# Kernel tuning notes

Measured on AMD Instinct MI355X. Metric: run time of the kernel, lower is better.

Reference implementation:

```python
import jax, jax.numpy as jnp
import numpy as np

B, S, D, H = 16, 512, 768, 12
DH = D // H


def setup_inputs() -> dict:
    key = jax.random.key(0)
    ks = jax.random.split(key, 12)
    hidden_states = jax.random.normal(ks[0], (B, S, D), dtype=jnp.float32)
    # additive padding mask: 0 for valid, -10000 for padded tail tokens
    lengths = jax.random.randint(ks[1], (B,), S // 2, S + 1)
    pad = (jnp.arange(S)[None, :] >= lengths[:, None]).astype(jnp.float32)
    attention_mask = (pad * -10000.0)[:, None, None, :]  # [B,1,1,S]
    # row-stochastic graph prior over codes
    pr = jax.random.uniform(ks[2], (B, S, S), dtype=jnp.float32)
    prior = pr / jnp.sum(pr, axis=-1, keepdims=True)
    s = 0.02
    params = dict(
        Wq=jax.random.normal(ks[3], (D, D)) * s, bq=jnp.zeros((D,)),
        Wk=jax.random.normal(ks[4], (D, D)) * s, bk=jnp.zeros((D,)),
        Wv=jax.random.normal(ks[5], (D, D)) * s, bv=jnp.zeros((D,)),
        Wg=jax.random.normal(ks[6], (D, 2)) * s, bg=jnp.zeros((2,)),
        Wo=jax.random.normal(ks[7], (D, D)) * s, bo=jnp.zeros((D,)),
        gamma=jnp.ones((D,)), beta=jnp.zeros((D,)),
    )
    return dict(hidden_states=hidden_states, attention_mask=attention_mask,
                prior=prior, **params)


def _layer_norm(x, gamma, beta, eps=1e-5):
    mu = jnp.mean(x, axis=-1, keepdims=True)
    var = jnp.mean(jnp.square(x - mu), axis=-1, keepdims=True)
    return (x - mu) * jax.lax.rsqrt(var + eps) * gamma + beta


def reference(hidden_states, attention_mask, prior,
              Wq, bq, Wk, bk, Wv, bv, Wg, bg, Wo, bo, gamma, beta):
    b, s, d = hidden_states.shape
    # project and split heads: [B,S,H,DH]
    q = (hidden_states @ Wq + bq).reshape(b, s, H, DH)
    k = (hidden_states @ Wk + bk).reshape(b, s, H, DH)
    v = (hidden_states @ Wv + bv).reshape(b, s, H, DH)
    scores = jnp.einsum('bshd,bthd->bhst', q, k) / jnp.sqrt(jnp.float32(DH))
    scores = scores + attention_mask  # broadcast [B,1,1,S]
    probs = jax.nn.softmax(scores, axis=-1)  # [B,H,S,S]
    # gate: avg-pool over valid tokens, softmax(linear/2)
    valid = (attention_mask.squeeze((1, 2)) == 0.0).astype(hidden_states.dtype)  # [B,S]
    denom = jnp.maximum(jnp.sum(valid, axis=1, keepdims=True), 1.0)
    h_pool = jnp.sum(hidden_states * valid[:, :, None], axis=1) / denom  # [B,D]
    gate = jax.nn.softmax((h_pool @ Wg + bg) / 2.0, axis=-1)  # [B,2]
    probs = probs * gate[:, 0, None, None, None] + prior[:, None, :, :] * gate[:, 1, None, None, None]
    ctx = jnp.einsum('bhst,bthd->bshd', probs, v).reshape(b, s, d)
    out = jax.nn.relu(ctx @ Wo + bo)
    out = _layer_norm(out + hidden_states, gamma, beta)
    return out
```

## Files before the change

kernel.cpp:

```cpp
#include <hip/hip_runtime.h>

#define NB_ 16
#define S_ 512
#define D_ 768
#define H_ 12
#define DH_ 64
#define QT_ 64
#define KT_ 128
#define LDQ_ 1536

typedef __attribute__((ext_vector_type(8))) short bf16x8;
typedef __attribute__((ext_vector_type(4))) float f32x4;
typedef unsigned short ushort_t;

__device__ __forceinline__ unsigned short f2bf(float f){
  unsigned int u = __float_as_uint(f);
  u += 0x7fffu + ((u >> 16) & 1u);
  return (unsigned short)(u >> 16);
}
__device__ __forceinline__ float bf2f(unsigned short s){
  return __uint_as_float(((unsigned int)s) << 16);
}
__device__ __forceinline__ unsigned int pack2(float a, float b){
  return (unsigned int)f2bf(a) | ((unsigned int)f2bf(b) << 16);
}
__device__ __forceinline__ void gld16(const ushort_t* g, ushort_t* l){
  __builtin_amdgcn_global_load_lds((const __attribute__((address_space(1))) unsigned int*)g,
                                   (__attribute__((address_space(3))) unsigned int*)l, 16, 0, 0);
}

__global__ __launch_bounds__(256) void k_setup(
    const float* __restrict__ hs, const float* __restrict__ mask, const float* __restrict__ prior,
    const float* __restrict__ W0, const float* __restrict__ W1,
    const float* __restrict__ W2, const float* __restrict__ W3,
    const float* __restrict__ b0, const float* __restrict__ b1, const float* __restrict__ b2,
    ushort_t* __restrict__ hsb, ushort_t* __restrict__ wt, float* __restrict__ bqkv,
    float* __restrict__ partial, float* __restrict__ pcnt, ushort_t* __restrict__ priorb)
{
  __shared__ float t[32][33];
  const int bx = blockIdx.x, tid = threadIdx.x;
  if (bx < 512){
    int chunk = bx & 31, b = bx >> 5;
    const float* mrow = mask + b * S_ + chunk * 16;
    const float* base = hs + ((size_t)b * S_ + chunk * 16) * D_;
    ushort_t* obase = hsb + ((size_t)b * S_ + chunk * 16) * D_;
    float a0 = 0.f, a1 = 0.f, a2 = 0.f, cnt = 0.f;
#pragma unroll 2
    for (int s = 0; s < 16; s++){
      const float* r = base + (size_t)s * D_;
      float x0 = r[tid], x1 = r[tid + 256], x2 = r[tid + 512];
      ushort_t* o = obase + (size_t)s * D_;
      o[tid] = f2bf(x0); o[tid + 256] = f2bf(x1); o[tid + 512] = f2bf(x2);
      if (mrow[s] == 0.0f){ a0 += x0; a1 += x1; a2 += x2; cnt += 1.0f; }
    }
    float* o = partial + (size_t)(b * 32 + chunk) * D_;
    o[tid] = a0; o[tid + 256] = a1; o[tid + 512] = a2;
    if (tid == 0) pcnt[b * 32 + chunk] = cnt;
  } else if (bx < 512 + 2304){
    int idx = bx - 512;
    int z = idx / 576, rem = idx - z * 576;
    int ky = rem / 24, nx = rem - ky * 24;
    const float* W = (z == 0) ? W0 : (z == 1) ? W1 : (z == 2) ? W2 : W3;
    ushort_t* o = wt + (size_t)z * D_ * D_;
    int j = tid & 31, i0 = tid >> 5;
    int kb = ky * 32, nb = nx * 32;
#pragma unroll
    for (int r = 0; r < 4; r++){
      int i = i0 + r * 8;
      t[i][j] = W[(size_t)(kb + i) * D_ + nb + j];
    }
    __syncthreads();
#pragma unroll
    for (int r = 0; r < 4; r++){
      int i = i0 + r * 8;
      o[(size_t)(nb + i) * D_ + kb + j] = f2bf(t[j][i]);
    }
  } else if (bx < 2825){
    int i = (bx - 2816) * 256 + tid;
    if (i < 3 * D_){
      float v = (i < D_) ? b0[i] : (i < 2 * D_) ? b1[i - D_] : b2[i - 2 * D_];
      bqkv[i] = v;
    }
  } else {
    size_t i = (size_t)(bx - 2825) * 4096 + (size_t)tid * 16;
    const float4* s4 = (const float4*)(prior + i);
    float4 f0 = s4[0], f1 = s4[1], f2 = s4[2], f3 = s4[3];
    uint4 p0, p1;
    p0.x = pack2(f0.x, f0.y); p0.y = pack2(f0.z, f0.w);
    p0.z = pack2(f1.x, f1.y); p0.w = pack2(f1.z, f1.w);
    p1.x = pack2(f2.x, f2.y); p1.y = pack2(f2.z, f2.w);
    p1.z = pack2(f3.x, f3.y); p1.w = pack2(f3.z, f3.w);
    *(uint4*)(priorb + i) = p0;
    *(uint4*)(priorb + i + 8) = p1;
  }
}

__global__ __launch_bounds__(256) void k_pool2(const float* __restrict__ partial, const float* __restrict__ pcnt,
                                               const float* __restrict__ Wg, const float* __restrict__ bg,
                                               float* __restrict__ gate){
  int b = blockIdx.x, tid = threadIdx.x;
  __shared__ float red[256];
  __shared__ float hp[768];
  float a0 = 0.f, a1 = 0.f, a2 = 0.f;
#pragma unroll
  for (int c = 0; c < 32; c++){
    const float* p = partial + (size_t)(b * 32 + c) * D_;
    a0 += p[tid]; a1 += p[tid + 256]; a2 += p[tid + 512];
  }
  float denom = 0.f;
#pragma unroll
  for (int c = 0; c < 32; c++) denom += pcnt[b * 32 + c];
  float inv = 1.0f / fmaxf(denom, 1.0f);
  hp[tid] = a0 * inv; hp[tid + 256] = a1 * inv; hp[tid + 512] = a2 * inv;
  __syncthreads();
  float p0 = 0.f, p1 = 0.f;
  for (int d = tid; d < D_; d += 256){ p0 += hp[d] * Wg[d * 2]; p1 += hp[d] * Wg[d * 2 + 1]; }
  red[tid] = p0; __syncthreads();
  for (int o = 128; o > 0; o >>= 1){ if (tid < o) red[tid] += red[tid + o]; __syncthreads(); }
  float z0 = red[0]; __syncthreads();
  red[tid] = p1; __syncthreads();
  for (int o = 128; o > 0; o >>= 1){ if (tid < o) red[tid] += red[tid + o]; __syncthreads(); }
  float z1 = red[0];
  if (tid == 0){
    z0 = (z0 + bg[0]) * 0.5f; z1 = (z1 + bg[1]) * 0.5f;
    float m = fmaxf(z0, z1);
    float e0 = __expf(z0 - m), e1 = __expf(z1 - m);
    float ssum = e0 + e1;
    gate[b * 2] = e0 / ssum; gate[b * 2 + 1] = e1 / ssum;
  }
}

template<int OUTBF16, int RELU, int RESID, int MAP, int VSPLIT>
__global__ __launch_bounds__(256, 2) void k_gemm_bt(
    const ushort_t* __restrict__ Am, long sA, int lda,
    const ushort_t* __restrict__ Bm, long sB, int ldb,
    void* __restrict__ Cp, long sC, int ldc, void* __restrict__ Cp2,
    const float* __restrict__ bias,
    const float* __restrict__ resid, float alpha, int K)
{
  __shared__ ushort_t As[2][128 * 64];
  __shared__ ushort_t Bs[2][128 * 64];
  int z, bm, bn;
  if (MAP == 2){ z = blockIdx.x; bm = blockIdx.y; bn = blockIdx.z; }
  else if (MAP == 1){ z = blockIdx.z; bm = blockIdx.x; bn = blockIdx.y; }
  else { z = blockIdx.z; bm = blockIdx.y; bn = blockIdx.x; }
  const ushort_t* Ab = Am + (size_t)z * sA;
  const ushort_t* Bb = Bm + (size_t)z * sB;
  const long coff = (long)z * sC;
  const int tid = threadIdx.x;
  const int m0 = bm * 128, n0 = bn * 128;
  const int wid = tid >> 6, lane = tid & 63;
  const int quad = lane >> 4, l16 = lane & 15;
  const int wm = wid >> 1, wn = wid & 1;
  const int sw = l16 & 7;

  auto stage = [&](int buf, int k0){
#pragma unroll
    for (int c = 0; c < 4; c++){
      int idx = tid + c * 256;
      int row = idx >> 3, p = idx & 7;
      int cg = p ^ (row & 7);
      gld16(Ab + (size_t)(m0 + row) * lda + k0 + cg * 8, &As[buf][idx * 8]);
    }
#pragma unroll
    for (int c = 0; c < 4; c++){
      int idx = tid + c * 256;
      int row = idx >> 3, p = idx & 7;
      int cg = p ^ (row & 7);
      gld16(Bb + (size_t)(n0 + row) * ldb + k0 + cg * 8, &Bs[buf][idx * 8]);
    }
  };

  f32x4 acc[4][4];
#pragma unroll
  for (int i = 0; i < 4; i++)
#pragma unroll
    for (int j = 0; j < 4; j++) acc[i][j] = (f32x4){0.f, 0.f, 0.f, 0.f};

  stage(0, 0);
  int cur = 0;
  for (int k0 = 0; k0 < K; k0 += 64){
    if (k0 + 64 < K){
      stage(cur ^ 1, k0 + 64);
      __builtin_amdgcn_sched_barrier(0);
      asm volatile("s_waitcnt vmcnt(8)" ::: "memory");
    } else {
      __builtin_amdgcn_sched_barrier(0);
      asm volatile("s_waitcnt vmcnt(0)" ::: "memory");
    }
    __builtin_amdgcn_sched_barrier(0);
    __builtin_amdgcn_s_barrier();
#pragma unroll
    for (int ks = 0; ks < 2; ks++){
      bf16x8 af[4], bfv[4];
#pragma unroll
      for (int mi = 0; mi < 4; mi++){
        int row = wm * 64 + mi * 16 + l16;
        af[mi] = *(const bf16x8*)(&As[cur][(row * 8 + ((ks * 4 + quad) ^ sw)) * 8]);
      }
#pragma unroll
      for (int ni = 0; ni < 4; ni++){
        int row = wn * 64 + ni * 16 + l16;
        bfv[ni] = *(const bf16x8*)(&Bs[cur][(row * 8 + ((ks * 4 + quad) ^ sw)) * 8]);
      }
      __builtin_amdgcn_s_setprio(1);
#pragma unroll
      for (int mi = 0; mi < 4; mi++)
#pragma unroll
        for (int ni = 0; ni < 4; ni++)
          acc[mi][ni] = __builtin_amdgcn_mfma_f32_16x16x32_bf16(af[mi], bfv[ni], acc[mi][ni], 0, 0, 0);
      __builtin_amdgcn_s_setprio(0);
    }
    __builtin_amdgcn_sched_barrier(0);
    __builtin_amdgcn_s_barrier();
    cur ^= 1;
  }

  if (VSPLIT && n0 >= 1536){
    ushort_t* vtp = (ushort_t*)Cp2;
    const int bb = m0 >> 9;
#pragma unroll
    for (int mi = 0; mi < 4; mi++){
#pragma unroll
      for (int ni = 0; ni < 4; ni++){
        int col = n0 + wn * 64 + ni * 16 + l16;
        float bcol = bias[col];
        int hh = (col - 1536) >> 6, dh = (col - 1536) & 63;
        int trow = (m0 & 511) + wm * 64 + mi * 16 + quad * 4;
        uint2 pk;
        pk.x = pack2(acc[mi][ni][0] + bcol, acc[mi][ni][1] + bcol);
        pk.y = pack2(acc[mi][ni][2] + bcol, acc[mi][ni][3] + bcol);
        *(uint2*)(vtp + ((size_t)(bb * H_ + hh) * DH_ + dh) * S_ + trow) = pk;
      }
    }
    return;
  }

#pragma unroll
  for (int mi = 0; mi < 4; mi++){
#pragma unroll
    for (int ni = 0; ni < 4; ni++){
      int col = n0 + wn * 64 + ni * 16 + l16;
      float bcol = bias ? bias[col] : 0.0f;
#pragma unroll
      for (int r = 0; r < 4; r++){
        int row = m0 + wm * 64 + mi * 16 + quad * 4 + r;
        float v = acc[mi][ni][r] * alpha + bcol;
        if (RELU) v = fmaxf(v, 0.0f);
        if (RESID) v += resid[(size_t)row * ldc + col];
        long idx = coff + (long)row * ldc + col;
        if (OUTBF16) ((ushort_t*)Cp)[idx] = f2bf(v);
        else         ((float*)Cp)[idx] = v;
      }
    }
  }
}

__global__ __launch_bounds__(256) void k_flash(
    const ushort_t* __restrict__ qkv,
    const ushort_t* __restrict__ vt,
    const ushort_t* __restrict__ priorctx,
    const float* __restrict__ mask,
    const float* __restrict__ gate,
    ushort_t* __restrict__ ctx)
{
  __shared__ ushort_t Ks[KT_ * 64];
  __shared__ ushort_t Vs[DH_ * 128];
  __shared__ ushort_t Ps[QT_ * 136];
  __shared__ float rs[QT_];
  const int z = blockIdx.x, b = z / H_, h = z - b * H_;
  const int q0 = blockIdx.y * QT_;
  const int tid = threadIdx.x;
  const int wid = tid >> 6, lane = tid & 63, quad = lane >> 4, l16 = lane & 15;

  bf16x8 bq[4][2];
#pragma unroll
  for (int ni = 0; ni < 4; ni++)
#pragma unroll
    for (int ks = 0; ks < 2; ks++)
      bq[ni][ks] = *(const bf16x8*)(qkv + ((size_t)(b * S_ + q0 + ni * 16 + l16)) * LDQ_
                                    + h * DH_ + ks * 32 + quad * 8);
  if (tid < QT_) rs[tid] = 0.f;

  f32x4 accv[4];
#pragma unroll
  for (int ni = 0; ni < 4; ni++) accv[ni] = (f32x4){0.f, 0.f, 0.f, 0.f};

  for (int t0 = 0; t0 < S_; t0 += KT_){
    if (mask[b * S_ + t0] != 0.0f) break;
#pragma unroll
    for (int c = 0; c < 4; c++){
      int idx = tid + c * 256;
      int row = idx >> 3, p = idx & 7;
      int cg = p ^ (row & 7);
      gld16(qkv + ((size_t)(b * S_ + t0 + row)) * LDQ_ + D_ + h * DH_ + cg * 8, &Ks[idx * 8]);
    }
#pragma unroll
    for (int c = 0; c < 4; c++){
      int idx = tid + c * 256;
      int row = idx >> 4, p = idx & 15;
      int cg = p ^ (row & 15);
      gld16(vt + (size_t)z * (DH_ * S_) + (size_t)row * S_ + t0 + cg * 8, &Vs[idx * 8]);
    }
    __syncthreads();

    f32x4 accs[2][4];
#pragma unroll
    for (int mi = 0; mi < 2; mi++)
#pragma unroll
      for (int ni = 0; ni < 4; ni++) accs[mi][ni] = (f32x4){0.f, 0.f, 0.f, 0.f};
#pragma unroll
    for (int ks = 0; ks < 2; ks++){
      bf16x8 ak[2];
#pragma unroll
      for (int mi = 0; mi < 2; mi++){
        int row = wid * 32 + mi * 16 + l16;
        ak[mi] = *(const bf16x8*)(&Ks[(row * 8 + ((ks * 4 + quad) ^ (l16 & 7))) * 8]);
      }
#pragma unroll
      for (int mi = 0; mi < 2; mi++)
#pragma unroll
        for (int ni = 0; ni < 4; ni++)
          accs[mi][ni] = __builtin_amdgcn_mfma_f32_16x16x32_bf16(ak[mi], bq[ni][ks], accs[mi][ni], 0, 0, 0);
    }

    float mv[2][4];
#pragma unroll
    for (int mi = 0; mi < 2; mi++)
#pragma unroll
      for (int r = 0; r < 4; r++)
        mv[mi][r] = mask[b * S_ + t0 + wid * 32 + mi * 16 + quad * 4 + r];
    float rowpart[4] = {0.f, 0.f, 0.f, 0.f};
#pragma unroll
    for (int mi = 0; mi < 2; mi++){
#pragma unroll
      for (int ni = 0; ni < 4; ni++){
        float e0 = __expf(accs[mi][ni][0] * 0.125f + mv[mi][0]);
        float e1 = __expf(accs[mi][ni][1] * 0.125f + mv[mi][1]);
        float e2 = __expf(accs[mi][ni][2] * 0.125f + mv[mi][2]);
        float e3 = __expf(accs[mi][ni][3] * 0.125f + mv[mi][3]);
        rowpart[ni] += (e0 + e1) + (e2 + e3);
        uint2 pk;
        pk.x = pack2(e0, e1);
        pk.y = pack2(e2, e3);
        *(uint2*)(&Ps[(ni * 16 + l16) * 136 + wid * 32 + mi * 16 + quad * 4]) = pk;
      }
    }
#pragma unroll
    for (int ni = 0; ni < 4; ni++){
      rowpart[ni] += __shfl_xor(rowpart[ni], 16);
      rowpart[ni] += __shfl_xor(rowpart[ni], 32);
    }
    if (lane < 16){
#pragma unroll
      for (int ni = 0; ni < 4; ni++) atomicAdd(&rs[ni * 16 + l16], rowpart[ni]);
    }
    __syncthreads();

#pragma unroll
    for (int ks = 0; ks < 4; ks++){
      bf16x8 ap = *(const bf16x8*)(&Ps[(wid * 16 + l16) * 136 + ks * 32 + quad * 8]);
#pragma unroll
      for (int ni = 0; ni < 4; ni++){
        bf16x8 bv8 = *(const bf16x8*)(&Vs[((ni * 16 + l16) * 16 + ((ks * 4 + quad) ^ l16)) * 8]);
        accv[ni] = __builtin_amdgcn_mfma_f32_16x16x32_bf16(ap, bv8, accv[ni], 0, 0, 0);
      }
    }
    __syncthreads();
  }

  const float g0 = gate[b * 2], g1 = gate[b * 2 + 1];
#pragma unroll
  for (int ni = 0; ni < 4; ni++){
#pragma unroll
    for (int r = 0; r < 4; r++){
      int q = wid * 16 + quad * 4 + r;
      int dh = ni * 16 + l16;
      float scl = g0 / rs[q];
      size_t idx = ((size_t)(b * S_ + q0 + q)) * D_ + h * DH_ + dh;
      float v = accv[ni][r] * scl + g1 * bf2f(priorctx[idx]);
      ctx[idx] = f2bf(v);
    }
  }
}

__global__ __launch_bounds__(256) void k_ln(float* __restrict__ out, const float* __restrict__ gamma,
                                            const float* __restrict__ beta){
  __shared__ float red[256];
  int row = blockIdx.x, tid = threadIdx.x;
  float* p = out + (size_t)row * D_;
  float x0 = p[tid], x1 = p[tid + 256], x2 = p[tid + 512];
  red[tid] = x0 + x1 + x2; __syncthreads();
  for (int o = 128; o > 0; o >>= 1){ if (tid < o) red[tid] += red[tid + o]; __syncthreads(); }
  float mu = red[0] * (1.0f / 768.0f);
  __syncthreads();
  float d0 = x0 - mu, d1 = x1 - mu, d2 = x2 - mu;
  red[tid] = d0 * d0 + d1 * d1 + d2 * d2; __syncthreads();
  for (int o = 128; o > 0; o >>= 1){ if (tid < o) red[tid] += red[tid + o]; __syncthreads(); }
  float rsv = rsqrtf(red[0] * (1.0f / 768.0f) + 1e-5f);
  p[tid]       = d0 * rsv * gamma[tid]       + beta[tid];
  p[tid + 256] = d1 * rsv * gamma[tid + 256] + beta[tid + 256];
  p[tid + 512] = d2 * rsv * gamma[tid + 512] + beta[tid + 512];
}

extern "C" void kernel_launch(void* const* d_in, const int* in_sizes, int n_in,
                              void* d_out, int out_size, void* d_ws, size_t ws_size,
                              hipStream_t stream){
  const float* hs    = (const float*)d_in[0];
  const float* mask  = (const float*)d_in[1];
  const float* prior = (const float*)d_in[2];
  const float* Wq = (const float*)d_in[3];  const float* bq = (const float*)d_in[4];
  const float* Wk = (const float*)d_in[5];  const float* bk = (const float*)d_in[6];
  const float* Wv = (const float*)d_in[7];  const float* bv = (const float*)d_in[8];
  const float* Wg = (const float*)d_in[9];  const float* bg = (const float*)d_in[10];
  const float* Wo = (const float*)d_in[11]; const float* bo = (const float*)d_in[12];
  const float* gamma = (const float*)d_in[13]; const float* beta = (const float*)d_in[14];
  float* out = (float*)d_out;

  size_t off = 0;
  auto alloc = [&](size_t bytes) -> char* {
    char* p = (char*)d_ws + off;
    off += (bytes + 255) & ~(size_t)255;
    return p;
  };
  const size_t HSD = (size_t)NB_ * S_ * D_;
  ushort_t* hsb     = (ushort_t*)alloc(HSD * 2);
  ushort_t* qkvb    = (ushort_t*)alloc(HSD * 2 * 2);
  ushort_t* vtb     = (ushort_t*)alloc(HSD * 2);
  ushort_t* wt      = (ushort_t*)alloc((size_t)4 * D_ * D_ * 2);
  ushort_t* priorctx= (ushort_t*)alloc(HSD * 2);
  ushort_t* ctx     = (ushort_t*)alloc(HSD * 2);
  float*    bqkv    = (float*)alloc((size_t)3 * D_ * 4);
  float*    gate    = (float*)alloc(256);
  float*    partial = (float*)alloc((size_t)NB_ * 32 * D_ * 4);
  float*    pcnt    = (float*)alloc((size_t)NB_ * 32 * 4);
  ushort_t* priorb  = ctx;

  k_setup<<<dim3(3849), 256, 0, stream>>>(hs, mask, prior, Wq, Wk, Wv, Wo, bq, bk, bv,
                                          hsb, wt, bqkv, partial, pcnt, priorb);
  k_pool2<<<dim3(NB_), 256, 0, stream>>>(partial, pcnt, Wg, bg, gate);
  k_gemm_bt<1, 0, 0, 1, 1><<<dim3(64, 18, 1), 256, 0, stream>>>(
      hsb, 0, D_, wt, 0, D_, qkvb, 0, LDQ_, vtb, bqkv, nullptr, 1.0f, D_);
  k_gemm_bt<1, 0, 0, 2, 0><<<dim3(16, 4, 6), 256, 0, stream>>>(
      priorb, (long)S_ * S_, S_, vtb, (long)H_ * DH_ * S_, S_,
      priorctx, (long)S_ * D_, D_, nullptr, nullptr, nullptr, 1.0f, S_);
  k_flash<<<dim3(NB_ * H_, S_ / QT_), 256, 0, stream>>>(
      qkvb, vtb, priorctx, mask, gate, ctx);
  k_gemm_bt<0, 1, 1, 1, 0><<<dim3(64, 6, 1), 256, 0, stream>>>(
      ctx, 0, D_, wt + 3 * (size_t)D_ * D_, 0, D_, out, 0, D_, nullptr, bo, hs, 1.0f, D_);
  k_ln<<<dim3(NB_ * S_), 256, 0, stream>>>(out, gamma, beta);
}
```

Baseline: 265.4 us.

## Replace QKV projection GEMM with 256x256-tile 8-wave pipelined kernel

```diff
diff --git a/kernel.cpp b/kernel.cpp
--- a/kernel.cpp
+++ b/kernel.cpp
@@ -256,6 +256,165 @@
   }
 }
 
+__global__ __launch_bounds__(512, 2) void k_gemm8_qkv(
+    const ushort_t* __restrict__ A,
+    const ushort_t* __restrict__ B,
+    ushort_t* __restrict__ Cq,
+    ushort_t* __restrict__ vt,
+    const float* __restrict__ bias)
+{
+  __shared__ ushort_t Al[2][2][256 * 32];
+  __shared__ ushort_t Bl[2][2][256 * 32];
+  const int tid = threadIdx.x;
+  const int m0 = blockIdx.x * 256, n0 = blockIdx.y * 256;
+  const int wid = tid >> 6, lane = tid & 63;
+  const int quad = lane >> 4, l16 = lane & 15;
+  const int wm = wid >> 2, wn = wid & 3;
+
+  const int i0c = tid, i1c = tid + 512;
+  const int r0 = i0c >> 2, c0 = (i0c & 3) ^ (r0 & 3);
+  const int r1 = i1c >> 2, c1 = (i1c & 3) ^ (r1 & 3);
+  const size_t a0 = (size_t)(m0 + r0) * 768 + c0 * 8;
+  const size_t a1 = (size_t)(m0 + r1) * 768 + c1 * 8;
+  const size_t b0 = (size_t)(n0 + r0) * 768 + c0 * 8;
+  const size_t b1 = (size_t)(n0 + r1) * 768 + c1 * 8;
+
+  auto stA = [&](int slot, int ks, int kt){
+    int ko = kt * 64 + ks * 32;
+    gld16(A + a0 + ko, &Al[slot][ks][i0c * 8]);
+    gld16(A + a1 + ko, &Al[slot][ks][i1c * 8]);
+  };
+  auto stB = [&](int slot, int ks, int kt){
+    int ko = kt * 64 + ks * 32;
+    gld16(B + b0 + ko, &Bl[slot][ks][i0c * 8]);
+    gld16(B + b1 + ko, &Bl[slot][ks][i1c * 8]);
+  };
+  auto rdA = [&](int slot, int ks, int mi) -> bf16x8 {
+    int row = wm * 128 + mi * 16 + l16;
+    return *(const bf16x8*)(&Al[slot][ks][(row * 4 + (quad ^ (row & 3))) * 8]);
+  };
+  auto rdB = [&](int slot, int ks, int ni) -> bf16x8 {
+    int row = wn * 64 + ni * 16 + l16;
+    return *(const bf16x8*)(&Bl[slot][ks][(row * 4 + (quad ^ (row & 3))) * 8]);
+  };
+
+  f32x4 acc[8][4];
+#pragma unroll
+  for (int i = 0; i < 8; i++)
+#pragma unroll
+    for (int j = 0; j < 4; j++) acc[i][j] = (f32x4){0.f, 0.f, 0.f, 0.f};
+
+  stA(0, 0, 0); stB(0, 0, 0); stA(0, 1, 0); stB(0, 1, 0);
+  stA(1, 0, 1); stB(1, 0, 1); stA(1, 1, 1);
+  __builtin_amdgcn_sched_barrier(0);
+  asm volatile("s_waitcnt vmcnt(6)" ::: "memory");
+  __builtin_amdgcn_sched_barrier(0);
+  __builtin_amdgcn_s_barrier();
+
+#pragma unroll 2
+  for (int t = 0; t < 12; ++t){
+    const int s = t & 1, o = s ^ 1;
+    bf16x8 aL[8], aH[8], bL[4], bH[4];
+#pragma unroll
+    for (int mi = 0; mi < 8; mi++) aL[mi] = rdA(s, 0, mi);
+#pragma unroll
+    for (int ni = 0; ni < 4; ni++) bL[ni] = rdB(s, 0, ni);
+    if (t + 1 < 12) stB(o, 1, t + 1);
+    __builtin_amdgcn_sched_barrier(0);
+    __builtin_amdgcn_s_barrier();
+    asm volatile("s_waitcnt lgkmcnt(0)" ::: "memory");
+    __builtin_amdgcn_sched_barrier(0);
+    __builtin_amdgcn_s_setprio(1);
+#pragma unroll
+    for (int mi = 0; mi < 4; mi++)
+#pragma unroll
+      for (int ni = 0; ni < 4; ni++)
+        acc[mi][ni] = __builtin_amdgcn_mfma_f32_16x16x32_bf16(aL[mi], bL[ni], acc[mi][ni], 0, 0, 0);
+    __builtin_amdgcn_s_setprio(0);
+    __builtin_amdgcn_sched_barrier(0);
+    __builtin_amdgcn_s_barrier();
+#pragma unroll
+    for (int ni = 0; ni < 4; ni++) bH[ni] = rdB(s, 1, ni);
+    if (t + 2 < 12) stA(s, 0, t + 2);
+    __builtin_amdgcn_sched_barrier(0);
+    __builtin_amdgcn_s_barrier();
+    asm volatile("s_waitcnt lgkmcnt(0)" ::: "memory");
+    __builtin_amdgcn_sched_barrier(0);
+    __builtin_amdgcn_s_setprio(1);
+#pragma unroll
+    for (int mi = 4; mi < 8; mi++)
+#pragma unroll
+      for (int ni = 0; ni < 4; ni++)
+        acc[mi][ni] = __builtin_amdgcn_mfma_f32_16x16x32_bf16(aL[mi], bL[ni], acc[mi][ni], 0, 0, 0);
+    __builtin_amdgcn_s_setprio(0);
+    __builtin_amdgcn_sched_barrier(0);
+    __builtin_amdgcn_s_barrier();
+#pragma unroll
+    for (int mi = 0; mi < 8; mi++) aH[mi] = rdA(s, 1, mi);
+    if (t + 2 < 12) stB(s, 0, t + 2);
+    __builtin_amdgcn_sched_barrier(0);
+    __builtin_amdgcn_s_barrier();
+    asm volatile("s_waitcnt lgkmcnt(0)" ::: "memory");
+    __builtin_amdgcn_sched_barrier(0);
+    __builtin_amdgcn_s_setprio(1);
+#pragma unroll
+    for (int mi = 0; mi < 4; mi++)
+#pragma unroll
+      for (int ni = 0; ni < 4; ni++)
+        acc[mi][ni] = __builtin_amdgcn_mfma_f32_16x16x32_bf16(aH[mi], bH[ni], acc[mi][ni], 0, 0, 0);
+    __builtin_amdgcn_s_setprio(0);
+    __builtin_amdgcn_sched_barrier(0);
+    __builtin_amdgcn_s_barrier();
+    if (t + 2 < 12) stA(s, 1, t + 2);
+    __builtin_amdgcn_sched_barrier(0);
+    __builtin_amdgcn_s_barrier();
+    __builtin_amdgcn_s_setprio(1);
+#pragma unroll
+    for (int mi = 4; mi < 8; mi++)
+#pragma unroll
+      for (int ni = 0; ni < 4; ni++)
+        acc[mi][ni] = __builtin_amdgcn_mfma_f32_16x16x32_bf16(aH[mi], bH[ni], acc[mi][ni], 0, 0, 0);
+    __builtin_amdgcn_s_setprio(0);
+    __builtin_amdgcn_sched_barrier(0);
+    if (t < 10) { asm volatile("s_waitcnt vmcnt(6)" ::: "memory"); }
+    else        { asm volatile("s_waitcnt vmcnt(0)" ::: "memory"); }
+    __builtin_amdgcn_sched_barrier(0);
+    __builtin_amdgcn_s_barrier();
+  }
+
+  if (n0 >= 1536){
+    const int bb = m0 >> 9;
+#pragma unroll
+    for (int mi = 0; mi < 8; mi++){
+#pragma unroll
+      for (int ni = 0; ni < 4; ni++){
+        int col = n0 + wn * 64 + ni * 16 + l16;
+        float bcol = bias[col];
+        int hh = (col - 1536) >> 6, dh = (col - 1536) & 63;
+        int trow = (m0 & 511) + wm * 128 + mi * 16 + quad * 4;
+        uint2 pk;
+        pk.x = pack2(acc[mi][ni][0] + bcol, acc[mi][ni][1] + bcol);
+        pk.y = pack2(acc[mi][ni][2] + bcol, acc[mi][ni][3] + bcol);
+        *(uint2*)(vt + ((size_t)(bb * H_ + hh) * DH_ + dh) * S_ + trow) = pk;
+      }
+    }
+    return;
+  }
+#pragma unroll
+  for (int mi = 0; mi < 8; mi++){
+#pragma unroll
+    for (int ni = 0; ni < 4; ni++){
+      int col = n0 + wn * 64 + ni * 16 + l16;
+      float bcol = bias[col];
+#pragma unroll
+      for (int r = 0; r < 4; r++){
+        int row = m0 + wm * 128 + mi * 16 + quad * 4 + r;
+        Cq[(size_t)row * LDQ_ + col] = f2bf(acc[mi][ni][r] + bcol);
+      }
+    }
+  }
+}
+
 __global__ __launch_bounds__(256) void k_flash(
     const ushort_t* __restrict__ qkv,
     const ushort_t* __restrict__ vt,
@@ -439,8 +598,7 @@
   k_setup<<<dim3(3849), 256, 0, stream>>>(hs, mask, prior, Wq, Wk, Wv, Wo, bq, bk, bv,
                                           hsb, wt, bqkv, partial, pcnt, priorb);
   k_pool2<<<dim3(NB_), 256, 0, stream>>>(partial, pcnt, Wg, bg, gate);
-  k_gemm_bt<1, 0, 0, 1, 1><<<dim3(64, 18, 1), 256, 0, stream>>>(
-      hsb, 0, D_, wt, 0, D_, qkvb, 0, LDQ_, vtb, bqkv, nullptr, 1.0f, D_);
+  k_gemm8_qkv<<<dim3(32, 9), 512, 0, stream>>>(hsb, wt, qkvb, vtb, bqkv);
   k_gemm_bt<1, 0, 0, 2, 0><<<dim3(16, 4, 6), 256, 0, stream>>>(
       priorb, (long)S_ * S_, S_, vtb, (long)H_ * DH_ * S_, S_,
       priorctx, (long)S_ * D_, D_, nullptr, nullptr, nullptr, 1.0f, S_);
```

New measurement: 274.4 us. 3.4% more time.

## Fuse prior@V product into flash attention epilogue, dropping separate GEMM

Applied to the files above, without the earlier changes.

```diff
diff --git a/kernel.cpp b/kernel.cpp
--- a/kernel.cpp
+++ b/kernel.cpp
@@ -256,10 +256,10 @@
   }
 }
 
-__global__ __launch_bounds__(256) void k_flash(
+__global__ __launch_bounds__(256, 3) void k_flash(
     const ushort_t* __restrict__ qkv,
     const ushort_t* __restrict__ vt,
-    const ushort_t* __restrict__ priorctx,
+    const ushort_t* __restrict__ priorb,
     const float* __restrict__ mask,
     const float* __restrict__ gate,
     ushort_t* __restrict__ ctx)
@@ -369,6 +369,23 @@
     __syncthreads();
   }
 
+  f32x4 accp[4];
+#pragma unroll
+  for (int ni = 0; ni < 4; ni++) accp[ni] = (f32x4){0.f, 0.f, 0.f, 0.f};
+  {
+    const ushort_t* pr = priorb + ((size_t)(b * S_ + q0 + wid * 16 + l16)) * S_;
+    const ushort_t* vb = vt + (size_t)z * (DH_ * S_);
+#pragma unroll 4
+    for (int ks = 0; ks < 16; ks++){
+      bf16x8 apc = *(const bf16x8*)(pr + ks * 32 + quad * 8);
+#pragma unroll
+      for (int ni = 0; ni < 4; ni++){
+        bf16x8 bpc = *(const bf16x8*)(vb + (size_t)(ni * 16 + l16) * S_ + ks * 32 + quad * 8);
+        accp[ni] = __builtin_amdgcn_mfma_f32_16x16x32_bf16(apc, bpc, accp[ni], 0, 0, 0);
+      }
+    }
+  }
+
   const float g0 = gate[b * 2], g1 = gate[b * 2 + 1];
 #pragma unroll
   for (int ni = 0; ni < 4; ni++){
@@ -378,7 +395,7 @@
       int dh = ni * 16 + l16;
       float scl = g0 / rs[q];
       size_t idx = ((size_t)(b * S_ + q0 + q)) * D_ + h * DH_ + dh;
-      float v = accv[ni][r] * scl + g1 * bf2f(priorctx[idx]);
+      float v = accv[ni][r] * scl + g1 * accp[ni][r];
       ctx[idx] = f2bf(v);
     }
   }
@@ -428,24 +445,20 @@
   ushort_t* qkvb    = (ushort_t*)alloc(HSD * 2 * 2);
   ushort_t* vtb     = (ushort_t*)alloc(HSD * 2);
   ushort_t* wt      = (ushort_t*)alloc((size_t)4 * D_ * D_ * 2);
-  ushort_t* priorctx= (ushort_t*)alloc(HSD * 2);
   ushort_t* ctx     = (ushort_t*)alloc(HSD * 2);
+  ushort_t* priorb  = (ushort_t*)alloc((size_t)NB_ * S_ * S_ * 2);
   float*    bqkv    = (float*)alloc((size_t)3 * D_ * 4);
   float*    gate    = (float*)alloc(256);
   float*    partial = (float*)alloc((size_t)NB_ * 32 * D_ * 4);
   float*    pcnt    = (float*)alloc((size_t)NB_ * 32 * 4);
-  ushort_t* priorb  = ctx;
 
   k_setup<<<dim3(3849), 256, 0, stream>>>(hs, mask, prior, Wq, Wk, Wv, Wo, bq, bk, bv,
                                           hsb, wt, bqkv, partial, pcnt, priorb);
   k_pool2<<<dim3(NB_), 256, 0, stream>>>(partial, pcnt, Wg, bg, gate);
   k_gemm_bt<1, 0, 0, 1, 1><<<dim3(64, 18, 1), 256, 0, stream>>>(
       hsb, 0, D_, wt, 0, D_, qkvb, 0, LDQ_, vtb, bqkv, nullptr, 1.0f, D_);
-  k_gemm_bt<1, 0, 0, 2, 0><<<dim3(16, 4, 6), 256, 0, stream>>>(
-      priorb, (long)S_ * S_, S_, vtb, (long)H_ * DH_ * S_, S_,
-      priorctx, (long)S_ * D_, D_, nullptr, nullptr, nullptr, 1.0f, S_);
   k_flash<<<dim3(NB_ * H_, S_ / QT_), 256, 0, stream>>>(
-      qkvb, vtb, priorctx, mask, gate, ctx);
+      qkvb, vtb, priorb, mask, gate, ctx);
   k_gemm_bt<0, 1, 1, 1, 0><<<dim3(64, 6, 1), 256, 0, stream>>>(
       ctx, 0, D_, wt + 3 * (size_t)D_ * D_, 0, D_, out, 0, D_, nullptr, bo, hs, 1.0f, D_);
   k_ln<<<dim3(NB_ * S_), 256, 0, stream>>>(out, gamma, beta);
```

Measured after the change: 295.6 us. 1.11x slower.
